# Kernel optimization log

Hardware: AMD Instinct MI355X
Metric: run time of the kernel (lower is better)

The kernel has to match this reference:

```python
import jax, jax.numpy as jnp
import numpy as np

E, T, H, I, K = 32, 2048, 1024, 512, 4


def setup_inputs() -> dict:
    key = jax.random.key(0)
    k1, k2, k3, k4, k5 = jax.random.split(key, 5)
    hidden_states = jax.random.normal(k1, (T, H), dtype=jnp.float32)
    top_k_index = jax.random.randint(k2, (T, K), 0, E)
    w = jax.random.uniform(k3, (T, K), dtype=jnp.float32)
    top_k_weights = w / jnp.sum(w, axis=-1, keepdims=True)  # router-like normalized weights
    gate_up_proj = jax.random.normal(k4, (E, 2 * I, H), dtype=jnp.float32) * 0.02
    down_proj = jax.random.normal(k5, (E, H, I), dtype=jnp.float32) * 0.02
    return {
        "hidden_states": hidden_states,
        "top_k_index": top_k_index,
        "top_k_weights": top_k_weights,
        "gate_up_proj": gate_up_proj,
        "down_proj": down_proj,
    }


def reference(hidden_states, top_k_index, top_k_weights, gate_up_proj, down_proj):
    # Faithful to the eager MoE dispatch loop: for each expert e, gather the
    # tokens routed to it, run gate/up/down SwiGLU, scale by routing weight,
    # and scatter-add into the output. Expressed as a scan over experts with a
    # per-token routing weight that is 0 for unrouted tokens (identical math:
    # index_add over (token, slot) pairs == sum_k where(idx==e, w, 0)).
    num_experts = gate_up_proj.shape[0]
    inter = down_proj.shape[2]

    def expert_step(acc, xs):
        gup_w, down_w, e = xs  # [2I, H], [H, I], scalar expert id
        # combined routing weight per token for this expert: [T]
        w_tok = jnp.sum(jnp.where(top_k_index == e, top_k_weights, 0.0), axis=1)
        gu = hidden_states @ gup_w.T              # [T, 2I]
        gate, up = gu[:, :inter], gu[:, inter:]
        h = jax.nn.silu(gate) * up                # [T, I]
        out = h @ down_w.T                        # [T, H]
        return acc + out * w_tok[:, None], None

    init = jnp.zeros_like(hidden_states)
    final_hidden_states, _ = jax.lax.scan(
        expert_step, init,
        (gate_up_proj, down_proj, jnp.arange(num_experts)),
    )
    return final_hidden_states
```

## Files before the change

kernel.cpp:

```cpp
#include <hip/hip_runtime.h>

#define NE 32
#define NT 2048
#define NH 1024
#define NI 512
#define NK 4
#define CAP 512

typedef __attribute__((ext_vector_type(8))) short short8;
typedef __attribute__((ext_vector_type(4))) float floatx4;

static __device__ __forceinline__ unsigned pk_bf16(float x, float y) {
#if __has_builtin(__builtin_amdgcn_cvt_pk_bf16_f32)
    typedef __attribute__((ext_vector_type(2))) __bf16 bf16x2;
    union { bf16x2 v; unsigned u; } c;
    c.v = __builtin_amdgcn_cvt_pk_bf16_f32(x, y);
    return c.u;
#else
    union { float f; unsigned u; } a, b;
    a.f = x; b.f = y;
    unsigned ua = (a.u + 0x7fffu + ((a.u >> 16) & 1u)) >> 16;
    unsigned ub = (b.u + 0x7fffu + ((b.u >> 16) & 1u)) >> 16;
    return (ua & 0xffffu) | (ub << 16);
#endif
}

static __device__ __forceinline__ short8 pack8(const float* p) {
    union { unsigned u[4]; short8 s; } c;
    c.u[0] = pk_bf16(p[0], p[1]);
    c.u[1] = pk_bf16(p[2], p[3]);
    c.u[2] = pk_bf16(p[4], p[5]);
    c.u[3] = pk_bf16(p[6], p[7]);
    return c.s;
}

static __device__ __forceinline__ unsigned short bf16_1(float x) {
    return (unsigned short)(pk_bf16(x, 0.f) & 0xffffu);
}

__global__ void route_kernel(const int* __restrict__ idx,
                             const float* __restrict__ w,
                             int* __restrict__ counts,
                             int* __restrict__ tok,
                             float* __restrict__ wgt) {
    int tid = blockIdx.x * blockDim.x + threadIdx.x;
    if (tid >= NT * NK) return;
    int e = idx[tid];
    int pos = atomicAdd(&counts[e], 1);
    if (pos < CAP) {
        tok[e * CAP + pos] = tid;
        wgt[e * CAP + pos] = w[tid];
    }
}

__global__ void cvt_hidden(const float* __restrict__ hidden,
                           unsigned short* __restrict__ hb16) {
    size_t i = (size_t)(blockIdx.x * 256 + threadIdx.x) * 8;
    float tmp[8];
    *(floatx4*)tmp       = *(const floatx4*)(hidden + i);
    *(floatx4*)(tmp + 4) = *(const floatx4*)(hidden + i + 4);
    *(short8*)(hb16 + i) = pack8(tmp);
}

__global__ __launch_bounds__(256) void gateup_mfma(
    const unsigned short* __restrict__ hb16,
    const float* __restrict__ gup,
    const int* __restrict__ counts,
    const int* __restrict__ tok,
    unsigned short* __restrict__ hbuf)
{
    int e = blockIdx.z;
    int cnt = counts[e];
    int m0 = blockIdx.y * 128;
    if (m0 >= cnt) return;
    int j0 = blockIdx.x * 64;

    __shared__ __align__(16) char smem[36864];
    __shared__ int tks[128];

    short (*As)[72] = (short(*)[72])smem;
    short (*Bs)[72] = (short(*)[72])(smem + 18432);
    float (*upb)[64][68] = (float(*)[64][68])smem;

    int tid = threadIdx.x;
    if (tid < 128) {
        int mi = m0 + tid;
        tks[tid] = tok[e * CAP + (mi < cnt ? mi : m0)];
    }
    __syncthreads();

    int arow_base = tid >> 3;
    int acol = (tid & 7) * 8;
    const unsigned short* ap[4];
#pragma unroll
    for (int p = 0; p < 4; p++)
        ap[p] = hb16 + (size_t)(tks[p * 32 + arow_base] >> 2) * NH + acol;

    int brow_base = tid >> 4;
    int bcol = (tid & 15) * 4;
    const float* gup_e = gup + (size_t)e * (2 * NI) * NH;
    const float* bp0 = gup_e + (size_t)(j0 + brow_base) * NH + bcol;
#define GUP_OFF(p) ((size_t)(p) * 16 * NH + ((p) >= 4 ? (size_t)(NI - 64) * NH : (size_t)0))

    int wave = tid >> 6, lane = tid & 63;
    int wm = wave >> 1;
    int wv = wave & 1;
    int lcol = lane & 15;
    int quad = lane >> 4;
    int lk = quad * 8;

    floatx4 acc[4][4];
#pragma unroll
    for (int a = 0; a < 4; a++)
#pragma unroll
        for (int b = 0; b < 4; b++) acc[a][b] = (floatx4){0.f, 0.f, 0.f, 0.f};

    short8 ra[4];
    float4 rb[8];
#pragma unroll
    for (int p = 0; p < 4; p++) ra[p] = *(const short8*)(ap[p]);
#pragma unroll
    for (int p = 0; p < 8; p++) rb[p] = *(const float4*)(bp0 + GUP_OFF(p));

    for (int h0 = 0; h0 < NH; h0 += 64) {
#pragma unroll
        for (int p = 0; p < 4; p++)
            *(short8*)&As[p * 32 + arow_base][acol] = ra[p];
#pragma unroll
        for (int p = 0; p < 8; p++) {
            uint2 u;
            u.x = pk_bf16(rb[p].x, rb[p].y);
            u.y = pk_bf16(rb[p].z, rb[p].w);
            *(uint2*)&Bs[p * 16 + brow_base][bcol] = u;
        }
        __syncthreads();
        int hn = h0 + 64;
        if (hn < NH) {
#pragma unroll
            for (int p = 0; p < 4; p++) ra[p] = *(const short8*)(ap[p] + hn);
#pragma unroll
            for (int p = 0; p < 8; p++) rb[p] = *(const float4*)(bp0 + GUP_OFF(p) + hn);
        }
#pragma unroll
        for (int ks = 0; ks < 2; ks++) {
            short8 af[4], bfr[4];
#pragma unroll
            for (int mt = 0; mt < 4; mt++)
                af[mt] = *(const short8*)&As[wm * 64 + mt * 16 + lcol][ks * 32 + lk];
#pragma unroll
            for (int nt = 0; nt < 4; nt++)
                bfr[nt] = *(const short8*)&Bs[wv * 64 + nt * 16 + lcol][ks * 32 + lk];
#pragma unroll
            for (int mt = 0; mt < 4; mt++)
#pragma unroll
                for (int nt = 0; nt < 4; nt++)
                    acc[mt][nt] = __builtin_amdgcn_mfma_f32_16x16x32_bf16(
                        af[mt], bfr[nt], acc[mt][nt], 0, 0, 0);
        }
        __syncthreads();
    }

    if (wv == 1) {
#pragma unroll
        for (int mt = 0; mt < 4; mt++)
#pragma unroll
            for (int nt = 0; nt < 4; nt++)
#pragma unroll
                for (int i = 0; i < 4; i++)
                    upb[wm][mt * 16 + quad * 4 + i][nt * 16 + lcol] = acc[mt][nt][i];
    }
    __syncthreads();
    if (wv == 0) {
#pragma unroll
        for (int mt = 0; mt < 4; mt++) {
#pragma unroll
            for (int i = 0; i < 4; i++) {
                int lm = mt * 16 + quad * 4 + i;
                int m = wm * 64 + lm;
                if (m0 + m < cnt) {
                    unsigned short* hp = hbuf + (size_t)tks[m] * NI + j0;
#pragma unroll
                    for (int nt = 0; nt < 4; nt++) {
                        float g = acc[mt][nt][i];
                        float u = upb[wm][lm][nt * 16 + lcol];
                        float h = g / (1.f + __expf(-g)) * u;
                        hp[nt * 16 + lcol] = bf16_1(h);
                    }
                }
            }
        }
    }
}

__global__ __launch_bounds__(256) void down_mfma(
    const unsigned short* __restrict__ hbuf,
    const float* __restrict__ down,
    const int* __restrict__ counts,
    const int* __restrict__ tok,
    const float* __restrict__ wgt,
    float* __restrict__ out)
{
    int e = blockIdx.z;
    int cnt = counts[e];
    int m0 = blockIdx.y * 128;
    if (m0 >= cnt) return;
    int n0 = blockIdx.x * 128;

    __shared__ __align__(16) short As[128][72];
    __shared__ __align__(16) short Bs[128][72];
    __shared__ int tks[128];
    __shared__ float wls[128];

    int tid = threadIdx.x;
    if (tid < 128) {
        int mi = m0 + tid;
        int src = e * CAP + (mi < cnt ? mi : m0);
        tks[tid] = tok[src];
        wls[tid] = wgt[src];
    }
    __syncthreads();

    int arow_base = tid >> 3;
    int acol = (tid & 7) * 8;
    const unsigned short* ap[4];
#pragma unroll
    for (int p = 0; p < 4; p++)
        ap[p] = hbuf + (size_t)tks[p * 32 + arow_base] * NI + acol;

    int brow_base = tid >> 4;
    int bcol = (tid & 15) * 4;
    const float* down_e = down + (size_t)e * NH * NI;
    const float* bp0 = down_e + (size_t)(n0 + brow_base) * NI + bcol;
#define DN_OFF(p) ((size_t)(p) * 16 * NI)

    int wave = tid >> 6, lane = tid & 63;
    int wm = wave >> 1, wn = wave & 1;
    int lcol = lane & 15;
    int quad = lane >> 4;
    int lk = quad * 8;

    floatx4 acc[4][4];
#pragma unroll
    for (int a = 0; a < 4; a++)
#pragma unroll
        for (int b = 0; b < 4; b++) acc[a][b] = (floatx4){0.f, 0.f, 0.f, 0.f};

    short8 ra[4];
    float4 rb[8];
#pragma unroll
    for (int p = 0; p < 4; p++) ra[p] = *(const short8*)(ap[p]);
#pragma unroll
    for (int p = 0; p < 8; p++) rb[p] = *(const float4*)(bp0 + DN_OFF(p));

    for (int i0 = 0; i0 < NI; i0 += 64) {
#pragma unroll
        for (int p = 0; p < 4; p++)
            *(short8*)&As[p * 32 + arow_base][acol] = ra[p];
#pragma unroll
        for (int p = 0; p < 8; p++) {
            uint2 u;
            u.x = pk_bf16(rb[p].x, rb[p].y);
            u.y = pk_bf16(rb[p].z, rb[p].w);
            *(uint2*)&Bs[p * 16 + brow_base][bcol] = u;
        }
        __syncthreads();
        int in = i0 + 64;
        if (in < NI) {
#pragma unroll
            for (int p = 0; p < 4; p++) ra[p] = *(const short8*)(ap[p] + in);
#pragma unroll
            for (int p = 0; p < 8; p++) rb[p] = *(const float4*)(bp0 + DN_OFF(p) + in);
        }
#pragma unroll
        for (int ks = 0; ks < 2; ks++) {
            short8 af[4], bfr[4];
#pragma unroll
            for (int mt = 0; mt < 4; mt++)
                af[mt] = *(const short8*)&As[wm * 64 + mt * 16 + lcol][ks * 32 + lk];
#pragma unroll
            for (int nt = 0; nt < 4; nt++)
                bfr[nt] = *(const short8*)&Bs[wn * 64 + nt * 16 + lcol][ks * 32 + lk];
#pragma unroll
            for (int mt = 0; mt < 4; mt++)
#pragma unroll
                for (int nt = 0; nt < 4; nt++)
                    acc[mt][nt] = __builtin_amdgcn_mfma_f32_16x16x32_bf16(
                        af[mt], bfr[nt], acc[mt][nt], 0, 0, 0);
        }
        __syncthreads();
    }

#pragma unroll
    for (int mt = 0; mt < 4; mt++)
#pragma unroll
        for (int i = 0; i < 4; i++) {
            int m = wm * 64 + mt * 16 + quad * 4 + i;
            if (m0 + m < cnt) {
                int t = tks[m] >> 2;
                float wl = wls[m];
                float* op = out + (size_t)t * NH + n0 + wn * 64;
#pragma unroll
                for (int nt = 0; nt < 4; nt++)
                    atomicAdd(op + nt * 16 + lcol, acc[mt][nt][i] * wl);
            }
        }
}

extern "C" void kernel_launch(void* const* d_in, const int* in_sizes, int n_in,
                              void* d_out, int out_size, void* d_ws, size_t ws_size,
                              hipStream_t stream) {
    const float* hidden = (const float*)d_in[0];
    const int*   tk_idx = (const int*)d_in[1];
    const float* tk_w   = (const float*)d_in[2];
    const float* gup    = (const float*)d_in[3];
    const float* down   = (const float*)d_in[4];
    float* out = (float*)d_out;

    char* ws = (char*)d_ws;
    int*            counts = (int*)ws;
    int*            tok    = (int*)(ws + 256);
    float*          wgt    = (float*)(ws + 256 + NE * CAP * 4);
    unsigned short* hb16   = (unsigned short*)(ws + 256 + 2 * NE * CAP * 4);
    unsigned short* hbuf   = (unsigned short*)(ws + 256 + 2 * NE * CAP * 4
                                               + (size_t)NT * NH * 2);

    hipMemsetAsync(counts, 0, 256, stream);
    hipMemsetAsync(out, 0, (size_t)NT * NH * sizeof(float), stream);

    route_kernel<<<(NT * NK + 255) / 256, 256, 0, stream>>>(tk_idx, tk_w, counts, tok, wgt);
    cvt_hidden<<<(NT * NH / 8) / 256, 256, 0, stream>>>(hidden, hb16);

    dim3 gridG(NI / 64, CAP / 128, NE);
    gateup_mfma<<<gridG, 256, 0, stream>>>(hb16, gup, counts, tok, hbuf);

    dim3 gridD(NH / 128, CAP / 128, NE);
    down_mfma<<<gridD, 256, 0, stream>>>(hbuf, down, counts, tok, wgt, out);
}
```

Measured before the change: 338.9 us.

## Halve GEMM N-tiles, split K pipeline, replace atomic scatter with pair-buffer reduction

Both expert GEMM kernels now use N-tiles half as wide (32 gate/up columns, 64 down columns). This doubles the number of active blocks and cuts accumulator registers, so launch_bounds can request 4 blocks per SM. The weight prefetch is split into two half-buffers alternating across 64-wide K steps, which lowers register pressure. When the workspace is large enough, the down kernel writes weighted results per (token, slot) pair into a buffer with plain stores, and a separate kernel sums the four slots. That removes the output memset and the float atomics, at the cost of an extra 32 MB round trip and reloading the A tile more often because N-tiles are smaller.

```diff
diff --git a/kernel.cpp b/kernel.cpp
--- a/kernel.cpp
+++ b/kernel.cpp
@@ -62,7 +62,7 @@
     *(short8*)(hb16 + i) = pack8(tmp);
 }
 
-__global__ __launch_bounds__(256) void gateup_mfma(
+__global__ __launch_bounds__(256, 4) void gateup_mfma(
     const unsigned short* __restrict__ hb16,
     const float* __restrict__ gup,
     const int* __restrict__ counts,
@@ -73,14 +73,14 @@
     int cnt = counts[e];
     int m0 = blockIdx.y * 128;
     if (m0 >= cnt) return;
-    int j0 = blockIdx.x * 64;
-
-    __shared__ __align__(16) char smem[36864];
+    int j0 = blockIdx.x * 32;
+
+    __shared__ __align__(16) char smem[27648];
     __shared__ int tks[128];
 
     short (*As)[72] = (short(*)[72])smem;
     short (*Bs)[72] = (short(*)[72])(smem + 18432);
-    float (*upb)[64][68] = (float(*)[64][68])smem;
+    float (*upb)[64][36] = (float(*)[64][36])smem;
 
     int tid = threadIdx.x;
     if (tid < 128) {
@@ -98,9 +98,9 @@
 
     int brow_base = tid >> 4;
     int bcol = (tid & 15) * 4;
-    const float* gup_e = gup + (size_t)e * (2 * NI) * NH;
-    const float* bp0 = gup_e + (size_t)(j0 + brow_base) * NH + bcol;
-#define GUP_OFF(p) ((size_t)(p) * 16 * NH + ((p) >= 4 ? (size_t)(NI - 64) * NH : (size_t)0))
+    const float* bp0 = gup + (size_t)e * (2 * NI) * NH
+                           + (size_t)(j0 + brow_base) * NH + bcol;
+#define GUP_OFF(p) ((size_t)(p) * 16 * NH + ((p) >= 2 ? (size_t)(NI - 32) * NH : (size_t)0))
 
     int wave = tid >> 6, lane = tid & 63;
     int wm = wave >> 1;
@@ -109,54 +109,80 @@
     int quad = lane >> 4;
     int lk = quad * 8;
 
-    floatx4 acc[4][4];
+    floatx4 acc[4][2];
 #pragma unroll
     for (int a = 0; a < 4; a++)
 #pragma unroll
-        for (int b = 0; b < 4; b++) acc[a][b] = (floatx4){0.f, 0.f, 0.f, 0.f};
+        for (int b = 0; b < 2; b++) acc[a][b] = (floatx4){0.f, 0.f, 0.f, 0.f};
 
     short8 ra[4];
-    float4 rb[8];
+    float4 rbA[4], rbB[4];
 #pragma unroll
     for (int p = 0; p < 4; p++) ra[p] = *(const short8*)(ap[p]);
 #pragma unroll
-    for (int p = 0; p < 8; p++) rb[p] = *(const float4*)(bp0 + GUP_OFF(p));
-
-    for (int h0 = 0; h0 < NH; h0 += 64) {
+    for (int p = 0; p < 4; p++) rbA[p] = *(const float4*)(bp0 + GUP_OFF(p));
+#pragma unroll
+    for (int p = 0; p < 4; p++) rbB[p] = *(const float4*)(bp0 + GUP_OFF(p) + 64);
+
+    auto commit = [&](short8* raq, float4* rbq) {
 #pragma unroll
         for (int p = 0; p < 4; p++)
-            *(short8*)&As[p * 32 + arow_base][acol] = ra[p];
-#pragma unroll
-        for (int p = 0; p < 8; p++) {
+            *(short8*)&As[p * 32 + arow_base][acol] = raq[p];
+#pragma unroll
+        for (int p = 0; p < 4; p++) {
             uint2 u;
-            u.x = pk_bf16(rb[p].x, rb[p].y);
-            u.y = pk_bf16(rb[p].z, rb[p].w);
+            u.x = pk_bf16(rbq[p].x, rbq[p].y);
+            u.y = pk_bf16(rbq[p].z, rbq[p].w);
             *(uint2*)&Bs[p * 16 + brow_base][bcol] = u;
         }
-        __syncthreads();
-        int hn = h0 + 64;
-        if (hn < NH) {
-#pragma unroll
-            for (int p = 0; p < 4; p++) ra[p] = *(const short8*)(ap[p] + hn);
-#pragma unroll
-            for (int p = 0; p < 8; p++) rb[p] = *(const float4*)(bp0 + GUP_OFF(p) + hn);
-        }
+    };
+    auto mfma_step = [&]() {
 #pragma unroll
         for (int ks = 0; ks < 2; ks++) {
-            short8 af[4], bfr[4];
+            short8 af[4], bfr[2];
 #pragma unroll
             for (int mt = 0; mt < 4; mt++)
                 af[mt] = *(const short8*)&As[wm * 64 + mt * 16 + lcol][ks * 32 + lk];
 #pragma unroll
-            for (int nt = 0; nt < 4; nt++)
-                bfr[nt] = *(const short8*)&Bs[wv * 64 + nt * 16 + lcol][ks * 32 + lk];
+            for (int nt = 0; nt < 2; nt++)
+                bfr[nt] = *(const short8*)&Bs[wv * 32 + nt * 16 + lcol][ks * 32 + lk];
 #pragma unroll
             for (int mt = 0; mt < 4; mt++)
 #pragma unroll
-                for (int nt = 0; nt < 4; nt++)
+                for (int nt = 0; nt < 2; nt++)
                     acc[mt][nt] = __builtin_amdgcn_mfma_f32_16x16x32_bf16(
                         af[mt], bfr[nt], acc[mt][nt], 0, 0, 0);
         }
+    };
+
+    for (int h0 = 0; h0 < NH; h0 += 128) {
+        commit(ra, rbA);
+        __syncthreads();
+        {
+            int ha = h0 + 64;
+#pragma unroll
+            for (int p = 0; p < 4; p++) ra[p] = *(const short8*)(ap[p] + ha);
+            int hb = h0 + 128;
+            if (hb < NH) {
+#pragma unroll
+                for (int p = 0; p < 4; p++) rbA[p] = *(const float4*)(bp0 + GUP_OFF(p) + hb);
+            }
+        }
+        mfma_step();
+        __syncthreads();
+
+        commit(ra, rbB);
+        __syncthreads();
+        {
+            int ha = h0 + 128;
+            if (ha < NH) {
+#pragma unroll
+                for (int p = 0; p < 4; p++) ra[p] = *(const short8*)(ap[p] + ha);
+#pragma unroll
+                for (int p = 0; p < 4; p++) rbB[p] = *(const float4*)(bp0 + GUP_OFF(p) + ha + 64);
+            }
+        }
+        mfma_step();
         __syncthreads();
     }
 
@@ -164,7 +190,7 @@
 #pragma unroll
         for (int mt = 0; mt < 4; mt++)
 #pragma unroll
-            for (int nt = 0; nt < 4; nt++)
+            for (int nt = 0; nt < 2; nt++)
 #pragma unroll
                 for (int i = 0; i < 4; i++)
                     upb[wm][mt * 16 + quad * 4 + i][nt * 16 + lcol] = acc[mt][nt][i];
@@ -180,7 +206,7 @@
                 if (m0 + m < cnt) {
                     unsigned short* hp = hbuf + (size_t)tks[m] * NI + j0;
 #pragma unroll
-                    for (int nt = 0; nt < 4; nt++) {
+                    for (int nt = 0; nt < 2; nt++) {
                         float g = acc[mt][nt][i];
                         float u = upb[wm][lm][nt * 16 + lcol];
                         float h = g / (1.f + __expf(-g)) * u;
@@ -192,22 +218,23 @@
     }
 }
 
-__global__ __launch_bounds__(256) void down_mfma(
+template<bool ATOMIC>
+__global__ __launch_bounds__(256, 4) void down_mfma(
     const unsigned short* __restrict__ hbuf,
-    const float* __restrict__ down,
+    const float* __restrict__ dwn,
     const int* __restrict__ counts,
     const int* __restrict__ tok,
     const float* __restrict__ wgt,
-    float* __restrict__ out)
+    float* __restrict__ outp)
 {
     int e = blockIdx.z;
     int cnt = counts[e];
     int m0 = blockIdx.y * 128;
     if (m0 >= cnt) return;
-    int n0 = blockIdx.x * 128;
+    int n0 = blockIdx.x * 64;
 
     __shared__ __align__(16) short As[128][72];
-    __shared__ __align__(16) short Bs[128][72];
+    __shared__ __align__(16) short Bs[64][72];
     __shared__ int tks[128];
     __shared__ float wls[128];
 
@@ -229,8 +256,7 @@
 
     int brow_base = tid >> 4;
     int bcol = (tid & 15) * 4;
-    const float* down_e = down + (size_t)e * NH * NI;
-    const float* bp0 = down_e + (size_t)(n0 + brow_base) * NI + bcol;
+    const float* bp0 = dwn + (size_t)e * NH * NI + (size_t)(n0 + brow_base) * NI + bcol;
 #define DN_OFF(p) ((size_t)(p) * 16 * NI)
 
     int wave = tid >> 6, lane = tid & 63;
@@ -239,54 +265,80 @@
     int quad = lane >> 4;
     int lk = quad * 8;
 
-    floatx4 acc[4][4];
+    floatx4 acc[4][2];
 #pragma unroll
     for (int a = 0; a < 4; a++)
 #pragma unroll
-        for (int b = 0; b < 4; b++) acc[a][b] = (floatx4){0.f, 0.f, 0.f, 0.f};
+        for (int b = 0; b < 2; b++) acc[a][b] = (floatx4){0.f, 0.f, 0.f, 0.f};
 
     short8 ra[4];
-    float4 rb[8];
+    float4 rbA[4], rbB[4];
 #pragma unroll
     for (int p = 0; p < 4; p++) ra[p] = *(const short8*)(ap[p]);
 #pragma unroll
-    for (int p = 0; p < 8; p++) rb[p] = *(const float4*)(bp0 + DN_OFF(p));
-
-    for (int i0 = 0; i0 < NI; i0 += 64) {
+    for (int p = 0; p < 4; p++) rbA[p] = *(const float4*)(bp0 + DN_OFF(p));
+#pragma unroll
+    for (int p = 0; p < 4; p++) rbB[p] = *(const float4*)(bp0 + DN_OFF(p) + 64);
+
+    auto commit = [&](short8* raq, float4* rbq) {
 #pragma unroll
         for (int p = 0; p < 4; p++)
-            *(short8*)&As[p * 32 + arow_base][acol] = ra[p];
-#pragma unroll
-        for (int p = 0; p < 8; p++) {
+            *(short8*)&As[p * 32 + arow_base][acol] = raq[p];
+#pragma unroll
+        for (int p = 0; p < 4; p++) {
             uint2 u;
-            u.x = pk_bf16(rb[p].x, rb[p].y);
-            u.y = pk_bf16(rb[p].z, rb[p].w);
+            u.x = pk_bf16(rbq[p].x, rbq[p].y);
+            u.y = pk_bf16(rbq[p].z, rbq[p].w);
             *(uint2*)&Bs[p * 16 + brow_base][bcol] = u;
         }
-        __syncthreads();
-        int in = i0 + 64;
-        if (in < NI) {
-#pragma unroll
-            for (int p = 0; p < 4; p++) ra[p] = *(const short8*)(ap[p] + in);
-#pragma unroll
-            for (int p = 0; p < 8; p++) rb[p] = *(const float4*)(bp0 + DN_OFF(p) + in);
-        }
+    };
+    auto mfma_step = [&]() {
 #pragma unroll
         for (int ks = 0; ks < 2; ks++) {
-            short8 af[4], bfr[4];
+            short8 af[4], bfr[2];
 #pragma unroll
             for (int mt = 0; mt < 4; mt++)
                 af[mt] = *(const short8*)&As[wm * 64 + mt * 16 + lcol][ks * 32 + lk];
 #pragma unroll
-            for (int nt = 0; nt < 4; nt++)
-                bfr[nt] = *(const short8*)&Bs[wn * 64 + nt * 16 + lcol][ks * 32 + lk];
+            for (int nt = 0; nt < 2; nt++)
+                bfr[nt] = *(const short8*)&Bs[wn * 32 + nt * 16 + lcol][ks * 32 + lk];
 #pragma unroll
             for (int mt = 0; mt < 4; mt++)
 #pragma unroll
-                for (int nt = 0; nt < 4; nt++)
+                for (int nt = 0; nt < 2; nt++)
                     acc[mt][nt] = __builtin_amdgcn_mfma_f32_16x16x32_bf16(
                         af[mt], bfr[nt], acc[mt][nt], 0, 0, 0);
         }
+    };
+
+    for (int i0 = 0; i0 < NI; i0 += 128) {
+        commit(ra, rbA);
+        __syncthreads();
+        {
+            int ia = i0 + 64;
+#pragma unroll
+            for (int p = 0; p < 4; p++) ra[p] = *(const short8*)(ap[p] + ia);
+            int ib = i0 + 128;
+            if (ib < NI) {
+#pragma unroll
+                for (int p = 0; p < 4; p++) rbA[p] = *(const float4*)(bp0 + DN_OFF(p) + ib);
+            }
+        }
+        mfma_step();
+        __syncthreads();
+
+        commit(ra, rbB);
+        __syncthreads();
+        {
+            int ia = i0 + 128;
+            if (ia < NI) {
+#pragma unroll
+                for (int p = 0; p < 4; p++) ra[p] = *(const short8*)(ap[p] + ia);
+#pragma unroll
+                for (int p = 0; p < 4; p++) rbB[p] = *(const float4*)(bp0 + DN_OFF(p) + ia + 64);
+            }
+        }
+        mfma_step();
         __syncthreads();
     }
 
@@ -296,14 +348,33 @@
         for (int i = 0; i < 4; i++) {
             int m = wm * 64 + mt * 16 + quad * 4 + i;
             if (m0 + m < cnt) {
-                int t = tks[m] >> 2;
                 float wl = wls[m];
-                float* op = out + (size_t)t * NH + n0 + wn * 64;
-#pragma unroll
-                for (int nt = 0; nt < 4; nt++)
-                    atomicAdd(op + nt * 16 + lcol, acc[mt][nt][i] * wl);
-            }
-        }
+                if (ATOMIC) {
+                    float* op = outp + (size_t)(tks[m] >> 2) * NH + n0 + wn * 32;
+#pragma unroll
+                    for (int nt = 0; nt < 2; nt++)
+                        atomicAdd(op + nt * 16 + lcol, acc[mt][nt][i] * wl);
+                } else {
+                    float* op = outp + (size_t)tks[m] * NH + n0 + wn * 32;
+#pragma unroll
+                    for (int nt = 0; nt < 2; nt++)
+                        op[nt * 16 + lcol] = acc[mt][nt][i] * wl;
+                }
+            }
+        }
+}
+
+__global__ void reduce_pairs(const float* __restrict__ pairbuf,
+                             float* __restrict__ out) {
+    int i = blockIdx.x * 256 + threadIdx.x;
+    int t = i / (NH / 4);
+    int c = (i - t * (NH / 4)) * 4;
+    const float* p = pairbuf + (size_t)t * NK * NH + c;
+    floatx4 a = *(const floatx4*)p;
+    a += *(const floatx4*)(p + NH);
+    a += *(const floatx4*)(p + 2 * NH);
+    a += *(const floatx4*)(p + 3 * NH);
+    *(floatx4*)(out + (size_t)t * NH + c) = a;
 }
 
 extern "C" void kernel_launch(void* const* d_in, const int* in_sizes, int n_in,
@@ -313,7 +384,7 @@
     const int*   tk_idx = (const int*)d_in[1];
     const float* tk_w   = (const float*)d_in[2];
     const float* gup    = (const float*)d_in[3];
-    const float* down   = (const float*)d_in[4];
+    const float* dwn    = (const float*)d_in[4];
     float* out = (float*)d_out;
 
     char* ws = (char*)d_ws;
@@ -323,16 +394,28 @@
     unsigned short* hb16   = (unsigned short*)(ws + 256 + 2 * NE * CAP * 4);
     unsigned short* hbuf   = (unsigned short*)(ws + 256 + 2 * NE * CAP * 4
                                                + (size_t)NT * NH * 2);
+    float*          pairbuf = (float*)(ws + 256 + 2 * NE * CAP * 4
+                                       + (size_t)NT * NH * 2
+                                       + (size_t)NT * NK * NI * 2);
+
+    size_t need = 256 + 2 * (size_t)NE * CAP * 4 + (size_t)NT * NH * 2
+                + (size_t)NT * NK * NI * 2 + (size_t)NT * NK * NH * 4;
+    bool pair_ok = ws_size >= need;
 
     hipMemsetAsync(counts, 0, 256, stream);
-    hipMemsetAsync(out, 0, (size_t)NT * NH * sizeof(float), stream);
 
     route_kernel<<<(NT * NK + 255) / 256, 256, 0, stream>>>(tk_idx, tk_w, counts, tok, wgt);
     cvt_hidden<<<(NT * NH / 8) / 256, 256, 0, stream>>>(hidden, hb16);
 
-    dim3 gridG(NI / 64, CAP / 128, NE);
+    dim3 gridG(NI / 32, CAP / 128, NE);
     gateup_mfma<<<gridG, 256, 0, stream>>>(hb16, gup, counts, tok, hbuf);
 
-    dim3 gridD(NH / 128, CAP / 128, NE);
-    down_mfma<<<gridD, 256, 0, stream>>>(hbuf, down, counts, tok, wgt, out);
-}
+    dim3 gridD(NH / 64, CAP / 128, NE);
+    if (pair_ok) {
+        down_mfma<false><<<gridD, 256, 0, stream>>>(hbuf, dwn, counts, tok, wgt, pairbuf);
+        reduce_pairs<<<(NT * NH / 4) / 256, 256, 0, stream>>>(pairbuf, out);
+    } else {
+        hipMemsetAsync(out, 0, (size_t)NT * NH * sizeof(float), stream);
+        down_mfma<true><<<gridD, 256, 0, stream>>>(hbuf, dwn, counts, tok, wgt, out);
+    }
+}
```

New measurement: 338.3 us. No clear change (-0.2%).

## Double-buffer MoE GEMMs with direct global-to-LDS loads and drop output atomics

Applied to the files above, without the earlier changes.

Both expert GEMM kernels now stage A (bf16) and B (raw fp32 weights) straight into LDS with global_load_lds, using two XOR-swizzled buffers. Explicit vmcnt waits and barriers let the next K-slice load overlap the MFMAs on the current one. The fp32-to-bf16 weight conversion moves to after the LDS read, which doubles B-tile LDS footprint and read traffic. Launch bounds now ask for 3 blocks per CU. When workspace allows, the down projection writes per-(token,slot) rows to a pair buffer and a separate reduction kernel sums the 4 slots. This replaces the output memset and fp32 atomics, at the cost of an extra 32 MB buffer round-trip.

```diff
diff --git a/kernel.cpp b/kernel.cpp
--- a/kernel.cpp
+++ b/kernel.cpp
@@ -9,6 +9,17 @@
 
 typedef __attribute__((ext_vector_type(8))) short short8;
 typedef __attribute__((ext_vector_type(4))) float floatx4;
+
+#define VMWAIT(n) asm volatile("s_waitcnt vmcnt(" #n ")" ::: "memory")
+#define FBAR() do { __builtin_amdgcn_sched_barrier(0);              \
+                    __builtin_amdgcn_s_barrier();                   \
+                    __builtin_amdgcn_sched_barrier(0); } while (0)
+
+static __device__ __forceinline__ void gload16(const void* g, void* l) {
+    __builtin_amdgcn_global_load_lds(
+        (const __attribute__((address_space(1))) unsigned int*)g,
+        (__attribute__((address_space(3))) unsigned int*)l, 16, 0, 0);
+}
 
 static __device__ __forceinline__ unsigned pk_bf16(float x, float y) {
 #if __has_builtin(__builtin_amdgcn_cvt_pk_bf16_f32)
@@ -62,7 +73,7 @@
     *(short8*)(hb16 + i) = pack8(tmp);
 }
 
-__global__ __launch_bounds__(256) void gateup_mfma(
+__global__ __launch_bounds__(256, 3) void gateup_mfma(
     const unsigned short* __restrict__ hb16,
     const float* __restrict__ gup,
     const int* __restrict__ counts,
@@ -75,12 +86,8 @@
     if (m0 >= cnt) return;
     int j0 = blockIdx.x * 64;
 
-    __shared__ __align__(16) char smem[36864];
+    __shared__ __align__(16) char smem[49152];
     __shared__ int tks[128];
-
-    short (*As)[72] = (short(*)[72])smem;
-    short (*Bs)[72] = (short(*)[72])(smem + 18432);
-    float (*upb)[64][68] = (float(*)[64][68])smem;
 
     int tid = threadIdx.x;
     if (tid < 128) {
@@ -89,25 +96,33 @@
     }
     __syncthreads();
 
-    int arow_base = tid >> 3;
-    int acol = (tid & 7) * 8;
-    const unsigned short* ap[4];
-#pragma unroll
-    for (int p = 0; p < 4; p++)
-        ap[p] = hb16 + (size_t)(tks[p * 32 + arow_base] >> 2) * NH + acol;
-
-    int brow_base = tid >> 4;
-    int bcol = (tid & 15) * 4;
+    int lane = tid & 63, wave = tid >> 6;
+
+    const unsigned short* aptr[2];
+#pragma unroll
+    for (int i = 0; i < 2; i++) {
+        int ar = wave * 32 + i * 16 + (lane >> 2);
+        aptr[i] = hb16 + (size_t)(tks[ar] >> 2) * NH + (lane & 3) * 8;
+    }
     const float* gup_e = gup + (size_t)e * (2 * NI) * NH;
-    const float* bp0 = gup_e + (size_t)(j0 + brow_base) * NH + bcol;
-#define GUP_OFF(p) ((size_t)(p) * 16 * NH + ((p) >= 4 ? (size_t)(NI - 64) * NH : (size_t)0))
-
-    int wave = tid >> 6, lane = tid & 63;
+    const float* bptr[4];
+#pragma unroll
+    for (int i = 0; i < 4; i++) {
+        int br = wave * 32 + i * 8 + (lane >> 3);
+        int gc = (lane & 7) ^ (br & 7);
+        int grow = (br < 64) ? (j0 + br) : (NI + j0 + (br - 64));
+        bptr[i] = gup_e + (size_t)grow * NH + gc * 4;
+    }
+
+    char* const A0 = smem;
+    char* const B0 = smem + 8192;
+    char* const A1 = smem + 24576;
+    char* const B1 = smem + 32768;
+
     int wm = wave >> 1;
     int wv = wave & 1;
     int lcol = lane & 15;
     int quad = lane >> 4;
-    int lk = quad * 8;
 
     floatx4 acc[4][4];
 #pragma unroll
@@ -115,51 +130,57 @@
 #pragma unroll
         for (int b = 0; b < 4; b++) acc[a][b] = (floatx4){0.f, 0.f, 0.f, 0.f};
 
-    short8 ra[4];
-    float4 rb[8];
-#pragma unroll
-    for (int p = 0; p < 4; p++) ra[p] = *(const short8*)(ap[p]);
-#pragma unroll
-    for (int p = 0; p < 8; p++) rb[p] = *(const float4*)(bp0 + GUP_OFF(p));
-
-    for (int h0 = 0; h0 < NH; h0 += 64) {
-#pragma unroll
-        for (int p = 0; p < 4; p++)
-            *(short8*)&As[p * 32 + arow_base][acol] = ra[p];
-#pragma unroll
-        for (int p = 0; p < 8; p++) {
-            uint2 u;
-            u.x = pk_bf16(rb[p].x, rb[p].y);
-            u.y = pk_bf16(rb[p].z, rb[p].w);
-            *(uint2*)&Bs[p * 16 + brow_base][bcol] = u;
-        }
-        __syncthreads();
-        int hn = h0 + 64;
-        if (hn < NH) {
-#pragma unroll
-            for (int p = 0; p < 4; p++) ra[p] = *(const short8*)(ap[p] + hn);
-#pragma unroll
-            for (int p = 0; p < 8; p++) rb[p] = *(const float4*)(bp0 + GUP_OFF(p) + hn);
-        }
-#pragma unroll
-        for (int ks = 0; ks < 2; ks++) {
-            short8 af[4], bfr[4];
-#pragma unroll
-            for (int mt = 0; mt < 4; mt++)
-                af[mt] = *(const short8*)&As[wm * 64 + mt * 16 + lcol][ks * 32 + lk];
+    auto stage = [&](char* dA, char* dB, int h) {
+#pragma unroll
+        for (int i = 0; i < 2; i++)
+            gload16(aptr[i] + h, dA + wave * 2048 + i * 1024);
+#pragma unroll
+        for (int i = 0; i < 4; i++)
+            gload16(bptr[i] + h, dB + wave * 4096 + i * 1024);
+    };
+    auto mfma_step = [&](const char* sA, const char* sB) {
+        short8 af[4], bfr[4];
+#pragma unroll
+        for (int mt = 0; mt < 4; mt++) {
+            int r = wm * 64 + mt * 16 + lcol;
+            af[mt] = *(const short8*)(sA + r * 64 + quad * 16);
+        }
+#pragma unroll
+        for (int nt = 0; nt < 4; nt++) {
+            int r = wv * 64 + nt * 16 + lcol;
+            const char* rb = sB + r * 128;
+            float4 lo = *(const float4*)(rb + (((quad * 2)     ^ (r & 7)) * 16));
+            float4 hi = *(const float4*)(rb + (((quad * 2 + 1) ^ (r & 7)) * 16));
+            union { unsigned u[4]; short8 s; } c;
+            c.u[0] = pk_bf16(lo.x, lo.y);
+            c.u[1] = pk_bf16(lo.z, lo.w);
+            c.u[2] = pk_bf16(hi.x, hi.y);
+            c.u[3] = pk_bf16(hi.z, hi.w);
+            bfr[nt] = c.s;
+        }
+#pragma unroll
+        for (int mt = 0; mt < 4; mt++)
 #pragma unroll
             for (int nt = 0; nt < 4; nt++)
-                bfr[nt] = *(const short8*)&Bs[wv * 64 + nt * 16 + lcol][ks * 32 + lk];
-#pragma unroll
-            for (int mt = 0; mt < 4; mt++)
-#pragma unroll
-                for (int nt = 0; nt < 4; nt++)
-                    acc[mt][nt] = __builtin_amdgcn_mfma_f32_16x16x32_bf16(
-                        af[mt], bfr[nt], acc[mt][nt], 0, 0, 0);
-        }
-        __syncthreads();
-    }
-
+                acc[mt][nt] = __builtin_amdgcn_mfma_f32_16x16x32_bf16(
+                    af[mt], bfr[nt], acc[mt][nt], 0, 0, 0);
+    };
+
+    stage(A0, B0, 0);
+    for (int kk = 0; kk < 32; kk += 2) {
+        stage(A1, B1, (kk + 1) * 32);
+        VMWAIT(6);
+        FBAR();
+        mfma_step(A0, B0);
+        FBAR();
+        if (kk + 2 < 32) { stage(A0, B0, (kk + 2) * 32); VMWAIT(6); }
+        else             { VMWAIT(0); }
+        FBAR();
+        mfma_step(A1, B1);
+        FBAR();
+    }
+
+    float (*upb)[64][68] = (float(*)[64][68])smem;
     if (wv == 1) {
 #pragma unroll
         for (int mt = 0; mt < 4; mt++)
@@ -192,13 +213,14 @@
     }
 }
 
-__global__ __launch_bounds__(256) void down_mfma(
+template<bool ATOMIC>
+__global__ __launch_bounds__(256, 3) void down_mfma(
     const unsigned short* __restrict__ hbuf,
-    const float* __restrict__ down,
+    const float* __restrict__ dwn,
     const int* __restrict__ counts,
     const int* __restrict__ tok,
     const float* __restrict__ wgt,
-    float* __restrict__ out)
+    float* __restrict__ outp)
 {
     int e = blockIdx.z;
     int cnt = counts[e];
@@ -206,8 +228,7 @@
     if (m0 >= cnt) return;
     int n0 = blockIdx.x * 128;
 
-    __shared__ __align__(16) short As[128][72];
-    __shared__ __align__(16) short Bs[128][72];
+    __shared__ __align__(16) char smem[49152];
     __shared__ int tks[128];
     __shared__ float wls[128];
 
@@ -220,24 +241,31 @@
     }
     __syncthreads();
 
-    int arow_base = tid >> 3;
-    int acol = (tid & 7) * 8;
-    const unsigned short* ap[4];
-#pragma unroll
-    for (int p = 0; p < 4; p++)
-        ap[p] = hbuf + (size_t)tks[p * 32 + arow_base] * NI + acol;
-
-    int brow_base = tid >> 4;
-    int bcol = (tid & 15) * 4;
-    const float* down_e = down + (size_t)e * NH * NI;
-    const float* bp0 = down_e + (size_t)(n0 + brow_base) * NI + bcol;
-#define DN_OFF(p) ((size_t)(p) * 16 * NI)
-
-    int wave = tid >> 6, lane = tid & 63;
+    int lane = tid & 63, wave = tid >> 6;
+
+    const unsigned short* aptr[2];
+#pragma unroll
+    for (int i = 0; i < 2; i++) {
+        int ar = wave * 32 + i * 16 + (lane >> 2);
+        aptr[i] = hbuf + (size_t)tks[ar] * NI + (lane & 3) * 8;
+    }
+    const float* dwn_e = dwn + (size_t)e * NH * NI;
+    const float* bptr[4];
+#pragma unroll
+    for (int i = 0; i < 4; i++) {
+        int br = wave * 32 + i * 8 + (lane >> 3);
+        int gc = (lane & 7) ^ (br & 7);
+        bptr[i] = dwn_e + (size_t)(n0 + br) * NI + gc * 4;
+    }
+
+    char* const A0 = smem;
+    char* const B0 = smem + 8192;
+    char* const A1 = smem + 24576;
+    char* const B1 = smem + 32768;
+
     int wm = wave >> 1, wn = wave & 1;
     int lcol = lane & 15;
     int quad = lane >> 4;
-    int lk = quad * 8;
 
     floatx4 acc[4][4];
 #pragma unroll
@@ -245,49 +273,54 @@
 #pragma unroll
         for (int b = 0; b < 4; b++) acc[a][b] = (floatx4){0.f, 0.f, 0.f, 0.f};
 
-    short8 ra[4];
-    float4 rb[8];
-#pragma unroll
-    for (int p = 0; p < 4; p++) ra[p] = *(const short8*)(ap[p]);
-#pragma unroll
-    for (int p = 0; p < 8; p++) rb[p] = *(const float4*)(bp0 + DN_OFF(p));
-
-    for (int i0 = 0; i0 < NI; i0 += 64) {
-#pragma unroll
-        for (int p = 0; p < 4; p++)
-            *(short8*)&As[p * 32 + arow_base][acol] = ra[p];
-#pragma unroll
-        for (int p = 0; p < 8; p++) {
-            uint2 u;
-            u.x = pk_bf16(rb[p].x, rb[p].y);
-            u.y = pk_bf16(rb[p].z, rb[p].w);
-            *(uint2*)&Bs[p * 16 + brow_base][bcol] = u;
-        }
-        __syncthreads();
-        int in = i0 + 64;
-        if (in < NI) {
-#pragma unroll
-            for (int p = 0; p < 4; p++) ra[p] = *(const short8*)(ap[p] + in);
-#pragma unroll
-            for (int p = 0; p < 8; p++) rb[p] = *(const float4*)(bp0 + DN_OFF(p) + in);
-        }
-#pragma unroll
-        for (int ks = 0; ks < 2; ks++) {
-            short8 af[4], bfr[4];
-#pragma unroll
-            for (int mt = 0; mt < 4; mt++)
-                af[mt] = *(const short8*)&As[wm * 64 + mt * 16 + lcol][ks * 32 + lk];
+    auto stage = [&](char* dA, char* dB, int h) {
+#pragma unroll
+        for (int i = 0; i < 2; i++)
+            gload16(aptr[i] + h, dA + wave * 2048 + i * 1024);
+#pragma unroll
+        for (int i = 0; i < 4; i++)
+            gload16(bptr[i] + h, dB + wave * 4096 + i * 1024);
+    };
+    auto mfma_step = [&](const char* sA, const char* sB) {
+        short8 af[4], bfr[4];
+#pragma unroll
+        for (int mt = 0; mt < 4; mt++) {
+            int r = wm * 64 + mt * 16 + lcol;
+            af[mt] = *(const short8*)(sA + r * 64 + quad * 16);
+        }
+#pragma unroll
+        for (int nt = 0; nt < 4; nt++) {
+            int r = wn * 64 + nt * 16 + lcol;
+            const char* rb = sB + r * 128;
+            float4 lo = *(const float4*)(rb + (((quad * 2)     ^ (r & 7)) * 16));
+            float4 hi = *(const float4*)(rb + (((quad * 2 + 1) ^ (r & 7)) * 16));
+            union { unsigned u[4]; short8 s; } c;
+            c.u[0] = pk_bf16(lo.x, lo.y);
+            c.u[1] = pk_bf16(lo.z, lo.w);
+            c.u[2] = pk_bf16(hi.x, hi.y);
+            c.u[3] = pk_bf16(hi.z, hi.w);
+            bfr[nt] = c.s;
+        }
+#pragma unroll
+        for (int mt = 0; mt < 4; mt++)
 #pragma unroll
             for (int nt = 0; nt < 4; nt++)
-                bfr[nt] = *(const short8*)&Bs[wn * 64 + nt * 16 + lcol][ks * 32 + lk];
-#pragma unroll
-            for (int mt = 0; mt < 4; mt++)
-#pragma unroll
-                for (int nt = 0; nt < 4; nt++)
-                    acc[mt][nt] = __builtin_amdgcn_mfma_f32_16x16x32_bf16(
-                        af[mt], bfr[nt], acc[mt][nt], 0, 0, 0);
-        }
-        __syncthreads();
+                acc[mt][nt] = __builtin_amdgcn_mfma_f32_16x16x32_bf16(
+                    af[mt], bfr[nt], acc[mt][nt], 0, 0, 0);
+    };
+
+    stage(A0, B0, 0);
+    for (int kk = 0; kk < 16; kk += 2) {
+        stage(A1, B1, (kk + 1) * 32);
+        VMWAIT(6);
+        FBAR();
+        mfma_step(A0, B0);
+        FBAR();
+        if (kk + 2 < 16) { stage(A0, B0, (kk + 2) * 32); VMWAIT(6); }
+        else             { VMWAIT(0); }
+        FBAR();
+        mfma_step(A1, B1);
+        FBAR();
     }
 
 #pragma unroll
@@ -296,14 +329,33 @@
         for (int i = 0; i < 4; i++) {
             int m = wm * 64 + mt * 16 + quad * 4 + i;
             if (m0 + m < cnt) {
-                int t = tks[m] >> 2;
                 float wl = wls[m];
-                float* op = out + (size_t)t * NH + n0 + wn * 64;
-#pragma unroll
-                for (int nt = 0; nt < 4; nt++)
-                    atomicAdd(op + nt * 16 + lcol, acc[mt][nt][i] * wl);
+                if (ATOMIC) {
+                    float* op = outp + (size_t)(tks[m] >> 2) * NH + n0 + wn * 64;
+#pragma unroll
+                    for (int nt = 0; nt < 4; nt++)
+                        atomicAdd(op + nt * 16 + lcol, acc[mt][nt][i] * wl);
+                } else {
+                    float* op = outp + (size_t)tks[m] * NH + n0 + wn * 64;
+#pragma unroll
+                    for (int nt = 0; nt < 4; nt++)
+                        op[nt * 16 + lcol] = acc[mt][nt][i] * wl;
+                }
             }
         }
+}
+
+__global__ void reduce_pairs(const float* __restrict__ pairbuf,
+                             float* __restrict__ out) {
+    int i = blockIdx.x * 256 + threadIdx.x;
+    int t = i / (NH / 4);
+    int c = (i - t * (NH / 4)) * 4;
+    const float* p = pairbuf + (size_t)t * NK * NH + c;
+    floatx4 a = *(const floatx4*)p;
+    a += *(const floatx4*)(p + NH);
+    a += *(const floatx4*)(p + 2 * NH);
+    a += *(const floatx4*)(p + 3 * NH);
+    *(floatx4*)(out + (size_t)t * NH + c) = a;
 }
 
 extern "C" void kernel_launch(void* const* d_in, const int* in_sizes, int n_in,
@@ -313,7 +365,7 @@
     const int*   tk_idx = (const int*)d_in[1];
     const float* tk_w   = (const float*)d_in[2];
     const float* gup    = (const float*)d_in[3];
-    const float* down   = (const float*)d_in[4];
+    const float* dwn    = (const float*)d_in[4];
     float* out = (float*)d_out;
 
     char* ws = (char*)d_ws;
@@ -323,9 +375,15 @@
     unsigned short* hb16   = (unsigned short*)(ws + 256 + 2 * NE * CAP * 4);
     unsigned short* hbuf   = (unsigned short*)(ws + 256 + 2 * NE * CAP * 4
                                                + (size_t)NT * NH * 2);
+    float*          pairbuf = (float*)(ws + 256 + 2 * NE * CAP * 4
+                                       + (size_t)NT * NH * 2
+                                       + (size_t)NT * NK * NI * 2);
+
+    size_t need = 256 + 2 * (size_t)NE * CAP * 4 + (size_t)NT * NH * 2
+                + (size_t)NT * NK * NI * 2 + (size_t)NT * NK * NH * 4;
+    bool pair_ok = ws_size >= need;
 
     hipMemsetAsync(counts, 0, 256, stream);
-    hipMemsetAsync(out, 0, (size_t)NT * NH * sizeof(float), stream);
 
     route_kernel<<<(NT * NK + 255) / 256, 256, 0, stream>>>(tk_idx, tk_w, counts, tok, wgt);
     cvt_hidden<<<(NT * NH / 8) / 256, 256, 0, stream>>>(hidden, hb16);
@@ -334,5 +392,11 @@
     gateup_mfma<<<gridG, 256, 0, stream>>>(hb16, gup, counts, tok, hbuf);
 
     dim3 gridD(NH / 128, CAP / 128, NE);
-    down_mfma<<<gridD, 256, 0, stream>>>(hbuf, down, counts, tok, wgt, out);
-}
+    if (pair_ok) {
+        down_mfma<false><<<gridD, 256, 0, stream>>>(hbuf, dwn, counts, tok, wgt, pairbuf);
+        reduce_pairs<<<(NT * NH / 4) / 256, 256, 0, stream>>>(pairbuf, out);
+    } else {
+        hipMemsetAsync(out, 0, (size_t)NT * NH * sizeof(float), stream);
+        down_mfma<true><<<gridD, 256, 0, stream>>>(hbuf, dwn, counts, tok, wgt, out);
+    }
+}
```

After: 376.7 us. +11.2%, slower.

## Double M-tile to 256 rows with 512 threads and replace atomics with pair-buffer reduction

Applied to the files above, without the earlier changes.

Both expert GEMM kernels now use 512-thread blocks covering 256 tokens per tile, so each weight tile converted from fp32 to bf16 is reused across twice as many rows and the fp32 weight traffic per token drops. The down projection writes per (token, slot) results into a workspace pair buffer without atomics, and a separate reduce kernel sums the four slots per token. This removes the output memset and atomic contention in exchange for a larger workspace write/read and an extra launch. There is a fallback to the atomic path when the workspace is too small.

```diff
diff --git a/kernel.cpp b/kernel.cpp
--- a/kernel.cpp
+++ b/kernel.cpp
@@ -62,7 +62,7 @@
     *(short8*)(hb16 + i) = pack8(tmp);
 }
 
-__global__ __launch_bounds__(256) void gateup_mfma(
+__global__ __launch_bounds__(512, 4) void gateup_mfma(
     const unsigned short* __restrict__ hb16,
     const float* __restrict__ gup,
     const int* __restrict__ counts,
@@ -71,43 +71,42 @@
 {
     int e = blockIdx.z;
     int cnt = counts[e];
-    int m0 = blockIdx.y * 128;
+    int m0 = blockIdx.y * 256;
     if (m0 >= cnt) return;
     int j0 = blockIdx.x * 64;
 
-    __shared__ __align__(16) char smem[36864];
-    __shared__ int tks[128];
-
-    short (*As)[72] = (short(*)[72])smem;
-    short (*Bs)[72] = (short(*)[72])(smem + 18432);
-    float (*upb)[64][68] = (float(*)[64][68])smem;
+    __shared__ __align__(16) short As[256][72];
+    __shared__ __align__(16) short Bs[128][72];
+    __shared__ int tks[256];
 
     int tid = threadIdx.x;
-    if (tid < 128) {
+    if (tid < 256) {
         int mi = m0 + tid;
         tks[tid] = tok[e * CAP + (mi < cnt ? mi : m0)];
     }
     __syncthreads();
 
-    int arow_base = tid >> 3;
+    int lane = tid & 63, wave = tid >> 6;
+    int wm = wave >> 1, wn = wave & 1;
+    int lcol = lane & 15, quad = lane >> 4;
+
+    int arow = tid >> 3;
     int acol = (tid & 7) * 8;
     const unsigned short* ap[4];
 #pragma unroll
     for (int p = 0; p < 4; p++)
-        ap[p] = hb16 + (size_t)(tks[p * 32 + arow_base] >> 2) * NH + acol;
-
-    int brow_base = tid >> 4;
+        ap[p] = hb16 + (size_t)(tks[p * 64 + arow] >> 2) * NH + acol;
+
+    int brow = tid >> 4;
     int bcol = (tid & 15) * 4;
     const float* gup_e = gup + (size_t)e * (2 * NI) * NH;
-    const float* bp0 = gup_e + (size_t)(j0 + brow_base) * NH + bcol;
-#define GUP_OFF(p) ((size_t)(p) * 16 * NH + ((p) >= 4 ? (size_t)(NI - 64) * NH : (size_t)0))
-
-    int wave = tid >> 6, lane = tid & 63;
-    int wm = wave >> 1;
-    int wv = wave & 1;
-    int lcol = lane & 15;
-    int quad = lane >> 4;
-    int lk = quad * 8;
+    const float* bptr[4];
+#pragma unroll
+    for (int p = 0; p < 4; p++) {
+        int r = p * 32 + brow;
+        int grow = (r < 64) ? (j0 + r) : (NI + j0 + (r - 64));
+        bptr[p] = gup_e + (size_t)grow * NH + bcol;
+    }
 
     floatx4 acc[4][4];
 #pragma unroll
@@ -116,22 +115,22 @@
         for (int b = 0; b < 4; b++) acc[a][b] = (floatx4){0.f, 0.f, 0.f, 0.f};
 
     short8 ra[4];
-    float4 rb[8];
+    float4 rb[4];
 #pragma unroll
     for (int p = 0; p < 4; p++) ra[p] = *(const short8*)(ap[p]);
 #pragma unroll
-    for (int p = 0; p < 8; p++) rb[p] = *(const float4*)(bp0 + GUP_OFF(p));
+    for (int p = 0; p < 4; p++) rb[p] = *(const float4*)(bptr[p]);
 
     for (int h0 = 0; h0 < NH; h0 += 64) {
 #pragma unroll
         for (int p = 0; p < 4; p++)
-            *(short8*)&As[p * 32 + arow_base][acol] = ra[p];
-#pragma unroll
-        for (int p = 0; p < 8; p++) {
+            *(short8*)&As[p * 64 + arow][acol] = ra[p];
+#pragma unroll
+        for (int p = 0; p < 4; p++) {
             uint2 u;
             u.x = pk_bf16(rb[p].x, rb[p].y);
             u.y = pk_bf16(rb[p].z, rb[p].w);
-            *(uint2*)&Bs[p * 16 + brow_base][bcol] = u;
+            *(uint2*)&Bs[p * 32 + brow][bcol] = u;
         }
         __syncthreads();
         int hn = h0 + 64;
@@ -139,17 +138,17 @@
 #pragma unroll
             for (int p = 0; p < 4; p++) ra[p] = *(const short8*)(ap[p] + hn);
 #pragma unroll
-            for (int p = 0; p < 8; p++) rb[p] = *(const float4*)(bp0 + GUP_OFF(p) + hn);
+            for (int p = 0; p < 4; p++) rb[p] = *(const float4*)(bptr[p] + hn);
         }
 #pragma unroll
         for (int ks = 0; ks < 2; ks++) {
             short8 af[4], bfr[4];
 #pragma unroll
             for (int mt = 0; mt < 4; mt++)
-                af[mt] = *(const short8*)&As[wm * 64 + mt * 16 + lcol][ks * 32 + lk];
+                af[mt] = *(const short8*)&As[wm * 64 + mt * 16 + lcol][ks * 32 + quad * 8];
 #pragma unroll
             for (int nt = 0; nt < 4; nt++)
-                bfr[nt] = *(const short8*)&Bs[wv * 64 + nt * 16 + lcol][ks * 32 + lk];
+                bfr[nt] = *(const short8*)&Bs[wn * 64 + nt * 16 + lcol][ks * 32 + quad * 8];
 #pragma unroll
             for (int mt = 0; mt < 4; mt++)
 #pragma unroll
@@ -160,59 +159,64 @@
         __syncthreads();
     }
 
-    if (wv == 1) {
-#pragma unroll
-        for (int mt = 0; mt < 4; mt++)
-#pragma unroll
-            for (int nt = 0; nt < 4; nt++)
-#pragma unroll
-                for (int i = 0; i < 4; i++)
-                    upb[wm][mt * 16 + quad * 4 + i][nt * 16 + lcol] = acc[mt][nt][i];
-    }
-    __syncthreads();
-    if (wv == 0) {
-#pragma unroll
-        for (int mt = 0; mt < 4; mt++) {
-#pragma unroll
-            for (int i = 0; i < 4; i++) {
-                int lm = mt * 16 + quad * 4 + i;
-                int m = wm * 64 + lm;
-                if (m0 + m < cnt) {
-                    unsigned short* hp = hbuf + (size_t)tks[m] * NI + j0;
-#pragma unroll
-                    for (int nt = 0; nt < 4; nt++) {
-                        float g = acc[mt][nt][i];
-                        float u = upb[wm][lm][nt * 16 + lcol];
-                        float h = g / (1.f + __expf(-g)) * u;
-                        hp[nt * 16 + lcol] = bf16_1(h);
+    float (*upb)[64][68] = (float(*)[64][68])As;
+    for (int half = 0; half < 2; half++) {
+        if ((wm >> 1) == half && wn == 1) {
+#pragma unroll
+            for (int mt = 0; mt < 4; mt++)
+#pragma unroll
+                for (int nt = 0; nt < 4; nt++)
+#pragma unroll
+                    for (int i = 0; i < 4; i++)
+                        upb[wm & 1][mt * 16 + quad * 4 + i][nt * 16 + lcol] = acc[mt][nt][i];
+        }
+        __syncthreads();
+        if ((wm >> 1) == half && wn == 0) {
+#pragma unroll
+            for (int mt = 0; mt < 4; mt++) {
+#pragma unroll
+                for (int i = 0; i < 4; i++) {
+                    int lm = mt * 16 + quad * 4 + i;
+                    int m = wm * 64 + lm;
+                    if (m0 + m < cnt) {
+                        unsigned short* hp = hbuf + (size_t)tks[m] * NI + j0;
+#pragma unroll
+                        for (int nt = 0; nt < 4; nt++) {
+                            float g = acc[mt][nt][i];
+                            float u = upb[wm & 1][lm][nt * 16 + lcol];
+                            float h = g / (1.f + __expf(-g)) * u;
+                            hp[nt * 16 + lcol] = bf16_1(h);
+                        }
                     }
                 }
             }
         }
-    }
-}
-
-__global__ __launch_bounds__(256) void down_mfma(
+        __syncthreads();
+    }
+}
+
+template<bool ATOMIC>
+__global__ __launch_bounds__(512, 4) void down_mfma(
     const unsigned short* __restrict__ hbuf,
-    const float* __restrict__ down,
+    const float* __restrict__ dwn,
     const int* __restrict__ counts,
     const int* __restrict__ tok,
     const float* __restrict__ wgt,
-    float* __restrict__ out)
+    float* __restrict__ outp)
 {
     int e = blockIdx.z;
     int cnt = counts[e];
-    int m0 = blockIdx.y * 128;
+    int m0 = blockIdx.y * 256;
     if (m0 >= cnt) return;
     int n0 = blockIdx.x * 128;
 
-    __shared__ __align__(16) short As[128][72];
+    __shared__ __align__(16) short As[256][72];
     __shared__ __align__(16) short Bs[128][72];
-    __shared__ int tks[128];
-    __shared__ float wls[128];
+    __shared__ int tks[256];
+    __shared__ float wls[256];
 
     int tid = threadIdx.x;
-    if (tid < 128) {
+    if (tid < 256) {
         int mi = m0 + tid;
         int src = e * CAP + (mi < cnt ? mi : m0);
         tks[tid] = tok[src];
@@ -220,24 +224,24 @@
     }
     __syncthreads();
 
-    int arow_base = tid >> 3;
+    int lane = tid & 63, wave = tid >> 6;
+    int wm = wave >> 1, wn = wave & 1;
+    int lcol = lane & 15, quad = lane >> 4;
+
+    int arow = tid >> 3;
     int acol = (tid & 7) * 8;
     const unsigned short* ap[4];
 #pragma unroll
     for (int p = 0; p < 4; p++)
-        ap[p] = hbuf + (size_t)tks[p * 32 + arow_base] * NI + acol;
-
-    int brow_base = tid >> 4;
+        ap[p] = hbuf + (size_t)tks[p * 64 + arow] * NI + acol;
+
+    int brow = tid >> 4;
     int bcol = (tid & 15) * 4;
-    const float* down_e = down + (size_t)e * NH * NI;
-    const float* bp0 = down_e + (size_t)(n0 + brow_base) * NI + bcol;
-#define DN_OFF(p) ((size_t)(p) * 16 * NI)
-
-    int wave = tid >> 6, lane = tid & 63;
-    int wm = wave >> 1, wn = wave & 1;
-    int lcol = lane & 15;
-    int quad = lane >> 4;
-    int lk = quad * 8;
+    const float* dwn_e = dwn + (size_t)e * NH * NI;
+    const float* bptr[4];
+#pragma unroll
+    for (int p = 0; p < 4; p++)
+        bptr[p] = dwn_e + (size_t)(n0 + p * 32 + brow) * NI + bcol;
 
     floatx4 acc[4][4];
 #pragma unroll
@@ -246,22 +250,22 @@
         for (int b = 0; b < 4; b++) acc[a][b] = (floatx4){0.f, 0.f, 0.f, 0.f};
 
     short8 ra[4];
-    float4 rb[8];
+    float4 rb[4];
 #pragma unroll
     for (int p = 0; p < 4; p++) ra[p] = *(const short8*)(ap[p]);
 #pragma unroll
-    for (int p = 0; p < 8; p++) rb[p] = *(const float4*)(bp0 + DN_OFF(p));
+    for (int p = 0; p < 4; p++) rb[p] = *(const float4*)(bptr[p]);
 
     for (int i0 = 0; i0 < NI; i0 += 64) {
 #pragma unroll
         for (int p = 0; p < 4; p++)
-            *(short8*)&As[p * 32 + arow_base][acol] = ra[p];
-#pragma unroll
-        for (int p = 0; p < 8; p++) {
+            *(short8*)&As[p * 64 + arow][acol] = ra[p];
+#pragma unroll
+        for (int p = 0; p < 4; p++) {
             uint2 u;
             u.x = pk_bf16(rb[p].x, rb[p].y);
             u.y = pk_bf16(rb[p].z, rb[p].w);
-            *(uint2*)&Bs[p * 16 + brow_base][bcol] = u;
+            *(uint2*)&Bs[p * 32 + brow][bcol] = u;
         }
         __syncthreads();
         int in = i0 + 64;
@@ -269,17 +273,17 @@
 #pragma unroll
             for (int p = 0; p < 4; p++) ra[p] = *(const short8*)(ap[p] + in);
 #pragma unroll
-            for (int p = 0; p < 8; p++) rb[p] = *(const float4*)(bp0 + DN_OFF(p) + in);
+            for (int p = 0; p < 4; p++) rb[p] = *(const float4*)(bptr[p] + in);
         }
 #pragma unroll
         for (int ks = 0; ks < 2; ks++) {
             short8 af[4], bfr[4];
 #pragma unroll
             for (int mt = 0; mt < 4; mt++)
-                af[mt] = *(const short8*)&As[wm * 64 + mt * 16 + lcol][ks * 32 + lk];
+                af[mt] = *(const short8*)&As[wm * 64 + mt * 16 + lcol][ks * 32 + quad * 8];
 #pragma unroll
             for (int nt = 0; nt < 4; nt++)
-                bfr[nt] = *(const short8*)&Bs[wn * 64 + nt * 16 + lcol][ks * 32 + lk];
+                bfr[nt] = *(const short8*)&Bs[wn * 64 + nt * 16 + lcol][ks * 32 + quad * 8];
 #pragma unroll
             for (int mt = 0; mt < 4; mt++)
 #pragma unroll
@@ -296,14 +300,33 @@
         for (int i = 0; i < 4; i++) {
             int m = wm * 64 + mt * 16 + quad * 4 + i;
             if (m0 + m < cnt) {
-                int t = tks[m] >> 2;
                 float wl = wls[m];
-                float* op = out + (size_t)t * NH + n0 + wn * 64;
-#pragma unroll
-                for (int nt = 0; nt < 4; nt++)
-                    atomicAdd(op + nt * 16 + lcol, acc[mt][nt][i] * wl);
+                if (ATOMIC) {
+                    float* op = outp + (size_t)(tks[m] >> 2) * NH + n0 + wn * 64;
+#pragma unroll
+                    for (int nt = 0; nt < 4; nt++)
+                        atomicAdd(op + nt * 16 + lcol, acc[mt][nt][i] * wl);
+                } else {
+                    float* op = outp + (size_t)tks[m] * NH + n0 + wn * 64;
+#pragma unroll
+                    for (int nt = 0; nt < 4; nt++)
+                        op[nt * 16 + lcol] = acc[mt][nt][i] * wl;
+                }
             }
         }
+}
+
+__global__ void reduce_pairs(const float* __restrict__ pairbuf,
+                             float* __restrict__ out) {
+    int i = blockIdx.x * 256 + threadIdx.x;
+    int t = i / (NH / 4);
+    int c = (i - t * (NH / 4)) * 4;
+    const float* p = pairbuf + (size_t)t * NK * NH + c;
+    floatx4 a = *(const floatx4*)p;
+    a += *(const floatx4*)(p + NH);
+    a += *(const floatx4*)(p + 2 * NH);
+    a += *(const floatx4*)(p + 3 * NH);
+    *(floatx4*)(out + (size_t)t * NH + c) = a;
 }
 
 extern "C" void kernel_launch(void* const* d_in, const int* in_sizes, int n_in,
@@ -313,7 +336,7 @@
     const int*   tk_idx = (const int*)d_in[1];
     const float* tk_w   = (const float*)d_in[2];
     const float* gup    = (const float*)d_in[3];
-    const float* down   = (const float*)d_in[4];
+    const float* dwn    = (const float*)d_in[4];
     float* out = (float*)d_out;
 
     char* ws = (char*)d_ws;
@@ -323,16 +346,28 @@
     unsigned short* hb16   = (unsigned short*)(ws + 256 + 2 * NE * CAP * 4);
     unsigned short* hbuf   = (unsigned short*)(ws + 256 + 2 * NE * CAP * 4
                                                + (size_t)NT * NH * 2);
+    float*          pairbuf = (float*)(ws + 256 + 2 * NE * CAP * 4
+                                       + (size_t)NT * NH * 2
+                                       + (size_t)NT * NK * NI * 2);
+
+    size_t need = 256 + 2 * (size_t)NE * CAP * 4 + (size_t)NT * NH * 2
+                + (size_t)NT * NK * NI * 2 + (size_t)NT * NK * NH * 4;
+    bool pair_ok = ws_size >= need;
 
     hipMemsetAsync(counts, 0, 256, stream);
-    hipMemsetAsync(out, 0, (size_t)NT * NH * sizeof(float), stream);
 
     route_kernel<<<(NT * NK + 255) / 256, 256, 0, stream>>>(tk_idx, tk_w, counts, tok, wgt);
     cvt_hidden<<<(NT * NH / 8) / 256, 256, 0, stream>>>(hidden, hb16);
 
-    dim3 gridG(NI / 64, CAP / 128, NE);
-    gateup_mfma<<<gridG, 256, 0, stream>>>(hb16, gup, counts, tok, hbuf);
-
-    dim3 gridD(NH / 128, CAP / 128, NE);
-    down_mfma<<<gridD, 256, 0, stream>>>(hbuf, down, counts, tok, wgt, out);
-}
+    dim3 gridG(NI / 64, CAP / 256, NE);
+    gateup_mfma<<<gridG, 512, 0, stream>>>(hb16, gup, counts, tok, hbuf);
+
+    dim3 gridD(NH / 128, CAP / 256, NE);
+    if (pair_ok) {
+        down_mfma<false><<<gridD, 512, 0, stream>>>(hbuf, dwn, counts, tok, wgt, pairbuf);
+        reduce_pairs<<<(NT * NH / 4) / 256, 256, 0, stream>>>(pairbuf, out);
+    } else {
+        hipMemsetAsync(out, 0, (size_t)NT * NH * sizeof(float), stream);
+        down_mfma<true><<<gridD, 512, 0, stream>>>(hbuf, dwn, counts, tok, wgt, out);
+    }
+}
```

After: 423.2 us. 1.25x slower.
